# Performance work log

Hardware: AMD Instinct MI355X
Metric: run time of the kernel (lower is better)

Reference implementation:

```python
import jax, jax.numpy as jnp
import numpy as np

HEADS = 16
DIM_HEAD = 64
RMS_EPS = 1.1920929e-07  # torch.finfo(float32).eps (torch RMSNorm eps=None default)
ROPE_THETA = 10000.0


def _rope(x):
    # x: [b, h, n, d]; rotary-embedding-torch style interleaved rotation
    n, d = x.shape[-2], x.shape[-1]
    inv_freq = 1.0 / (ROPE_THETA ** (jnp.arange(0, d, 2, dtype=jnp.float32) / d))
    t = jnp.arange(n, dtype=jnp.float32)
    freqs = t[:, None] * inv_freq[None, :]              # [n, d/2]
    cos = jnp.repeat(jnp.cos(freqs), 2, axis=-1)        # [n, d] interleaved
    sin = jnp.repeat(jnp.sin(freqs), 2, axis=-1)
    x1 = x[..., ::2]
    x2 = x[..., 1::2]
    rot = jnp.stack((-x2, x1), axis=-1).reshape(x.shape)  # rotate_half, interleaved pairs
    return x * cos + rot * sin


def setup_inputs() -> dict:
    key = jax.random.key(0)
    ks = jax.random.split(key, 6)
    b, n, dim = 2, 2048, 1024
    tokens = jax.random.normal(ks[0], (b, n, dim), dtype=jnp.float32)
    norm_weight = jnp.ones((dim,), dtype=jnp.float32)
    wq = jax.random.normal(ks[1], (dim, dim), dtype=jnp.float32) * 0.02
    wk = jax.random.normal(ks[2], (dim, dim), dtype=jnp.float32) * 0.02
    wv = jax.random.normal(ks[3], (dim, dim), dtype=jnp.float32) * 0.02
    wo = jax.random.normal(ks[4], (dim, dim), dtype=jnp.float32) * 0.02
    return {"tokens": tokens, "norm_weight": norm_weight, "wq": wq, "wk": wk, "wv": wv, "wo": wo}


def reference(tokens, norm_weight, wq, wk, wv, wo):
    b, n, dim = tokens.shape
    # RMSNorm (elementwise affine)
    x = tokens * jax.lax.rsqrt(jnp.mean(tokens * tokens, axis=-1, keepdims=True) + RMS_EPS)
    x = x * norm_weight
    # QKV projections (torch Linear: x @ W.T), split heads: b n (h d) -> b h n d
    def split(y):
        return y.reshape(b, n, HEADS, DIM_HEAD).transpose(0, 2, 1, 3)
    q = split(x @ wq.T) * (DIM_HEAD ** -0.5)
    k = split(x @ wk.T)
    v = split(x @ wv.T)
    # rotary embedding (no kv cache -> same positions for q and k)
    q = _rope(q)
    k = _rope(k)
    sim = jnp.einsum('bhid,bhjd->bhij', q, k)
    causal = jnp.triu(jnp.ones((n, n), dtype=bool), k=1)
    sim = jnp.where(causal, -jnp.finfo(sim.dtype).max, sim)
    attn = jax.nn.softmax(sim, axis=-1)
    out = jnp.einsum('bhij,bhjd->bhid', attn, v)
    out = out.transpose(0, 2, 1, 3).reshape(b, n, dim)  # merge heads
    return out @ wo.T
```

## Files before the change

kernel.cpp:

```cpp
#include <hip/hip_runtime.h>

typedef __bf16 bf16x8 __attribute__((ext_vector_type(8)));
typedef float f32x4 __attribute__((ext_vector_type(4)));

#define DIM 1024
#define NSEQ 2048

#define GL2LDS(g, l) __builtin_amdgcn_global_load_lds( \
    (const __attribute__((address_space(1))) void*)(g), \
    (__attribute__((address_space(3))) void*)(l), 16, 0, 0)

#define MFMA16(a, b, c) __builtin_amdgcn_mfma_f32_16x16x32_bf16(a, b, c, 0, 0, 0)

__global__ __launch_bounds__(256) void cvt_kernel(const float* __restrict__ s,
                                                  __bf16* __restrict__ d) {
    int i = (blockIdx.x * 256 + threadIdx.x) * 4;
    float4 f = *(const float4*)(s + i);
    union { uint2 u; __bf16 h[4]; } p;
    p.h[0] = (__bf16)f.x; p.h[1] = (__bf16)f.y;
    p.h[2] = (__bf16)f.z; p.h[3] = (__bf16)f.w;
    *(uint2*)(d + i) = p.u;
}

__global__ __launch_bounds__(256) void cvt3_kernel(const float* __restrict__ wq,
                                                   const float* __restrict__ wk,
                                                   const float* __restrict__ wv,
                                                   __bf16* __restrict__ dq,
                                                   __bf16* __restrict__ dk,
                                                   __bf16* __restrict__ dv,
                                                   int* __restrict__ counters) {
    if (blockIdx.x == 0 && blockIdx.y == 0 && threadIdx.x < 8)
        counters[threadIdx.x] = 0;
    const float* s = blockIdx.y == 0 ? wq : (blockIdx.y == 1 ? wk : wv);
    __bf16*      d = blockIdx.y == 0 ? dq : (blockIdx.y == 1 ? dk : dv);
    int i = (blockIdx.x * 256 + threadIdx.x) * 4;
    float4 f = *(const float4*)(s + i);
    union { uint2 u; __bf16 h[4]; } p;
    p.h[0] = (__bf16)f.x; p.h[1] = (__bf16)f.y;
    p.h[2] = (__bf16)f.z; p.h[3] = (__bf16)f.w;
    *(uint2*)(d + i) = p.u;
}

__global__ __launch_bounds__(256) void rmsnorm_kernel(const float* __restrict__ x,
                                                      const float* __restrict__ g,
                                                      __bf16* __restrict__ o) {
    int row = blockIdx.x;
    int t = threadIdx.x;
    float4 xv = ((const float4*)(x + (size_t)row * DIM))[t];
    float ss = xv.x*xv.x + xv.y*xv.y + xv.z*xv.z + xv.w*xv.w;
    #pragma unroll
    for (int off = 32; off; off >>= 1) ss += __shfl_xor(ss, off, 64);
    __shared__ float red[4];
    if ((t & 63) == 0) red[t >> 6] = ss;
    __syncthreads();
    ss = red[0] + red[1] + red[2] + red[3];
    float r = rsqrtf(ss * (1.0f / 1024.0f) + 1.1920929e-07f);
    float4 gv = ((const float4*)g)[t];
    union { uint2 u; __bf16 h[4]; } p;
    p.h[0] = (__bf16)(xv.x * r * gv.x);
    p.h[1] = (__bf16)(xv.y * r * gv.y);
    p.h[2] = (__bf16)(xv.z * r * gv.z);
    p.h[3] = (__bf16)(xv.w * r * gv.w);
    *(uint2*)(o + (size_t)row * DIM + t * 4) = p.u;
}

__global__ __launch_bounds__(256) void rope_kernel(__bf16* __restrict__ qb,
                                                   __bf16* __restrict__ kb) {
    int bid = blockIdx.x;
    __bf16* x = (bid & 1) ? kb : qb;
    int gid = (bid >> 1) * 256 + threadIdx.x;
    int row = gid >> 9;
    int pr = gid & 511;
    int pos = row & (NSEQ - 1);
    int dp = pr & 31;
    float inv = __expf(-(float)dp * (9.210340371976184f / 32.0f));
    float ang = (float)pos * inv;
    float sn, cs;
    sincosf(ang, &sn, &cs);
    size_t off = (size_t)row * DIM + pr * 2;
    union { unsigned int u; __bf16 h[2]; } p;
    p.u = *(const unsigned int*)(x + off);
    float x1 = (float)p.h[0], x2 = (float)p.h[1];
    p.h[0] = (__bf16)(x1 * cs - x2 * sn);
    p.h[1] = (__bf16)(x2 * cs + x1 * sn);
    *(unsigned int*)(x + off) = p.u;
}

template <typename CT>
__device__ __forceinline__ void gemm_body(const __bf16* __restrict__ A,
                                          const __bf16* __restrict__ B,
                                          CT* __restrict__ C,
                                          int mb, int nb, int ldc, float scale,
                                          __bf16* As, __bf16* Bs) {
    int t = threadIdx.x;
    int w = t >> 6, l = t & 63;
    int wm = (w >> 1) * 64, wn = (w & 1) * 64;
    int lrow = l & 15, lq = l >> 4;
    f32x4 acc[4][4] = {};

    int srow = w * 32 + (l >> 3);
    int sc8 = (l & 7) * 8;
    const __bf16* gA = A + (size_t)(mb * 128 + srow) * 1024 + sc8;
    const __bf16* gB = B + (size_t)(nb * 128 + srow) * 1024 + sc8;
    __bf16* lA = As + (size_t)(w * 32) * 64;
    __bf16* lB = Bs + (size_t)(w * 32) * 64;

    for (int kt = 0; kt < 16; ++kt) {
        int k0 = kt * 64;
        #pragma unroll
        for (int c = 0; c < 4; ++c) {
            GL2LDS(gA + (size_t)c * 8 * 1024 + k0, lA + c * 8 * 64);
            GL2LDS(gB + (size_t)c * 8 * 1024 + k0, lB + c * 8 * 64);
        }
        __syncthreads();
        #pragma unroll
        for (int ch = 0; ch < 2; ++ch) {
            bf16x8 af[4], bfr[4];
            #pragma unroll
            for (int i = 0; i < 4; ++i)
                af[i] = *(const bf16x8*)&As[(wm + i * 16 + lrow) * 64 + ch * 32 + lq * 8];
            #pragma unroll
            for (int i = 0; i < 4; ++i)
                bfr[i] = *(const bf16x8*)&Bs[(wn + i * 16 + lrow) * 64 + ch * 32 + lq * 8];
            #pragma unroll
            for (int rt = 0; rt < 4; ++rt)
                #pragma unroll
                for (int ct = 0; ct < 4; ++ct)
                    acc[rt][ct] = MFMA16(af[rt], bfr[ct], acc[rt][ct]);
        }
        __syncthreads();
    }
    #pragma unroll
    for (int rt = 0; rt < 4; ++rt)
        #pragma unroll
        for (int ct = 0; ct < 4; ++ct)
            #pragma unroll
            for (int r = 0; r < 4; ++r) {
                int row = mb * 128 + wm + rt * 16 + lq * 4 + r;
                int col = nb * 128 + wn + ct * 16 + lrow;
                C[(size_t)row * ldc + col] = (CT)(acc[rt][ct][r] * scale);
            }
}

__global__ __launch_bounds__(256) void qkv_kernel(const __bf16* __restrict__ x,
                                                  const __bf16* __restrict__ wq,
                                                  const __bf16* __restrict__ wk,
                                                  const __bf16* __restrict__ wv,
                                                  __bf16* __restrict__ qb,
                                                  __bf16* __restrict__ kb,
                                                  __bf16* __restrict__ vtb) {
    __shared__ __bf16 As[128 * 64];
    __shared__ __bf16 Bs[128 * 64];
    int bm = blockIdx.x, bn = blockIdx.y, z = blockIdx.z;
    if (z == 0)      gemm_body<__bf16>(x,  wq, qb,  bm, bn, 1024,
                                       0.125f * 1.44269504088896340736f, As, Bs);
    else if (z == 1) gemm_body<__bf16>(x,  wk, kb,  bm, bn, 1024, 1.0f,   As, Bs);
    else             gemm_body<__bf16>(wv, x,  vtb, bn, bm, 4096, 1.0f,   As, Bs);
}

__global__ __launch_bounds__(256) void wo_kernel(const __bf16* __restrict__ A,
                                                 const __bf16* __restrict__ B,
                                                 float* __restrict__ C) {
    __shared__ __bf16 As[128 * 64];
    __shared__ __bf16 Bs[128 * 64];
    gemm_body<float>(A, B, C, blockIdx.x, blockIdx.y, 1024, 1.0f, As, Bs);
}

__global__ __launch_bounds__(256) void attn_kernel(const __bf16* __restrict__ q,
                                                   const __bf16* __restrict__ kk,
                                                   const __bf16* __restrict__ vt,
                                                   __bf16* __restrict__ o,
                                                   int* __restrict__ counters) {
    int xcd = blockIdx.x & 7;
    int t = threadIdx.x;
    int w = t >> 6, l = t & 63;
    int lrow = l & 15, lq = l >> 4;

    __shared__ __bf16 Ps[4][32 * 76];
    __bf16* pw = Ps[w];

    for (;;) {
        int it = 0;
        if (l == 0) it = atomicAdd(&counters[xcd], 1);
        it = __shfl(it, 0, 64);
        if (it >= 256) break;
        int qq = 63 - (it >> 2);
        int bh = xcd * 4 + (it & 3);
        int h = bh & 15;
        int b = bh >> 4;
        int rowbase = b * NSEQ;
        int JT = qq >> 1;

        const __bf16* kbase = kk + (size_t)rowbase * DIM + h * 64;
        const __bf16* vbase = vt + (size_t)(h * 64) * 4096 + b * 2048;

        bf16x8 qf[2][2];
        #pragma unroll
        for (int g = 0; g < 2; ++g) {
            const __bf16* qp = q + (size_t)(rowbase + qq * 32 + g * 16 + lrow) * DIM + h * 64;
            qf[g][0] = *(const bf16x8*)(qp + lq * 8);
            qf[g][1] = *(const bf16x8*)(qp + 32 + lq * 8);
        }

        f32x4 oacc[2][4] = {};
        float m_r[2] = {-1e30f, -1e30f};
        float l_r[2] = {0.0f, 0.0f};

        bf16x8 kA[8], kB[8], vA[8], vB[8];
        #pragma unroll
        for (int ct = 0; ct < 4; ++ct) {
            const __bf16* kp = kbase + (size_t)(ct * 16 + lrow) * DIM;
            kA[ct * 2]     = *(const bf16x8*)(kp + lq * 8);
            kA[ct * 2 + 1] = *(const bf16x8*)(kp + 32 + lq * 8);
            const __bf16* vp = vbase + (size_t)(ct * 16 + lrow) * 4096;
            vA[ct * 2]     = *(const bf16x8*)(vp + lq * 8);
            vA[ct * 2 + 1] = *(const bf16x8*)(vp + 32 + lq * 8);
        }

        auto trip = [&](bf16x8 (&kc)[8], bf16x8 (&kn)[8],
                        bf16x8 (&vc)[8], bf16x8 (&vn)[8], int jt) {
            f32x4 st[2][4];
            #pragma unroll
            for (int ct = 0; ct < 4; ++ct)
                #pragma unroll
                for (int g = 0; g < 2; ++g) {
                    f32x4 z = {};
                    z = MFMA16(kc[ct * 2],     qf[g][0], z);
                    z = MFMA16(kc[ct * 2 + 1], qf[g][1], z);
                    st[g][ct] = z;
                }
            if (jt < JT) {
                int j1 = (jt + 1) * 64;
                #pragma unroll
                for (int ct = 0; ct < 4; ++ct) {
                    const __bf16* kp = kbase + (size_t)(j1 + ct * 16 + lrow) * DIM;
                    kn[ct * 2]     = *(const bf16x8*)(kp + lq * 8);
                    kn[ct * 2 + 1] = *(const bf16x8*)(kp + 32 + lq * 8);
                    const __bf16* vp = vbase + (size_t)(ct * 16 + lrow) * 4096 + j1;
                    vn[ct * 2]     = *(const bf16x8*)(vp + lq * 8);
                    vn[ct * 2 + 1] = *(const bf16x8*)(vp + 32 + lq * 8);
                }
            }
            if (jt == JT) {
                #pragma unroll
                for (int g = 0; g < 2; ++g) {
                    int qr = qq * 32 + g * 16 + lrow - JT * 64;
                    #pragma unroll
                    for (int ct = 0; ct < 4; ++ct)
                        #pragma unroll
                        for (int r = 0; r < 4; ++r)
                            if (ct * 16 + lq * 4 + r > qr) st[g][ct][r] = -3.0e38f;
                }
            }
            #pragma unroll
            for (int g = 0; g < 2; ++g) {
                float m0 = fmaxf(fmaxf(st[g][0][0], st[g][0][1]), fmaxf(st[g][0][2], st[g][0][3]));
                float m1 = fmaxf(fmaxf(st[g][1][0], st[g][1][1]), fmaxf(st[g][1][2], st[g][1][3]));
                float m2 = fmaxf(fmaxf(st[g][2][0], st[g][2][1]), fmaxf(st[g][2][2], st[g][2][3]));
                float m3 = fmaxf(fmaxf(st[g][3][0], st[g][3][1]), fmaxf(st[g][3][2], st[g][3][3]));
                float mx = fmaxf(fmaxf(m0, m1), fmaxf(m2, m3));
                mx = fmaxf(mx, __shfl_xor(mx, 16, 64));
                mx = fmaxf(mx, __shfl_xor(mx, 32, 64));
                if (!__all(mx - m_r[g] <= 8.0f)) {
                    float mnew = fmaxf(m_r[g], mx);
                    float alpha = __builtin_amdgcn_exp2f(m_r[g] - mnew);
                    l_r[g] *= alpha;
                    #pragma unroll
                    for (int ct = 0; ct < 4; ++ct)
                        #pragma unroll
                        for (int r = 0; r < 4; ++r) oacc[g][ct][r] *= alpha;
                    m_r[g] = mnew;
                }
                float ps = 0.0f;
                #pragma unroll
                for (int ct = 0; ct < 4; ++ct)
                    #pragma unroll
                    for (int r = 0; r < 4; ++r) {
                        float p = __builtin_amdgcn_exp2f(st[g][ct][r] - m_r[g]);
                        st[g][ct][r] = p;
                        ps += p;
                    }
                ps += __shfl_xor(ps, 16, 64);
                ps += __shfl_xor(ps, 32, 64);
                l_r[g] += ps;
            }
            #pragma unroll
            for (int g = 0; g < 2; ++g)
                #pragma unroll
                for (int ct = 0; ct < 4; ++ct) {
                    union { uint2 u; __bf16 h4[4]; } pk;
                    #pragma unroll
                    for (int r = 0; r < 4; ++r) pk.h4[r] = (__bf16)st[g][ct][r];
                    *(uint2*)&pw[(g * 16 + lrow) * 76 + ct * 16 + lq * 4] = pk.u;
                }
            bf16x8 pb[2][2];
            #pragma unroll
            for (int g = 0; g < 2; ++g) {
                pb[g][0] = *(const bf16x8*)&pw[(g * 16 + lrow) * 76 + lq * 8];
                pb[g][1] = *(const bf16x8*)&pw[(g * 16 + lrow) * 76 + 32 + lq * 8];
            }
            #pragma unroll
            for (int ct = 0; ct < 4; ++ct)
                #pragma unroll
                for (int g = 0; g < 2; ++g) {
                    oacc[g][ct] = MFMA16(vc[ct * 2],     pb[g][0], oacc[g][ct]);
                    oacc[g][ct] = MFMA16(vc[ct * 2 + 1], pb[g][1], oacc[g][ct]);
                }
        };

        int jt = 0;
        for (;;) {
            trip(kA, kB, vA, vB, jt);
            if (jt == JT) break;
            ++jt;
            trip(kB, kA, vB, vA, jt);
            if (jt == JT) break;
            ++jt;
        }

        #pragma unroll
        for (int g = 0; g < 2; ++g) {
            float rcp = 1.0f / l_r[g];
            const size_t orow = (size_t)(rowbase + qq * 32 + g * 16 + lrow) * DIM + h * 64;
            #pragma unroll
            for (int ct = 0; ct < 4; ++ct) {
                union { uint2 u; __bf16 h4[4]; } pk;
                #pragma unroll
                for (int r = 0; r < 4; ++r) pk.h4[r] = (__bf16)(oacc[g][ct][r] * rcp);
                *(uint2*)(o + orow + ct * 16 + lq * 4) = pk.u;
            }
        }
    }
}

extern "C" void kernel_launch(void* const* d_in, const int* in_sizes, int n_in,
                              void* d_out, int out_size, void* d_ws, size_t ws_size,
                              hipStream_t stream) {
    const float* tokens = (const float*)d_in[0];
    const float* gamma  = (const float*)d_in[1];
    const float* wq = (const float*)d_in[2];
    const float* wk = (const float*)d_in[3];
    const float* wv = (const float*)d_in[4];
    const float* wo = (const float*)d_in[5];

    __bf16* ws  = (__bf16*)d_ws;
    __bf16* x   = ws;
    __bf16* qb  = x   + (size_t)4096 * 1024;
    __bf16* kb  = qb  + (size_t)4096 * 1024;
    __bf16* vtb = kb  + (size_t)4096 * 1024;
    __bf16* ao  = x;
    __bf16* wob = qb;
    float*  out = (float*)d_out;

    __bf16* wqb = (__bf16*)d_out;
    __bf16* wkb = wqb + (size_t)1024 * 1024;
    __bf16* wvb = wkb + (size_t)1024 * 1024;
    int* counters = (int*)((char*)d_out + (size_t)8 * 1024 * 1024);

    cvt3_kernel<<<dim3(1024, 3), 256, 0, stream>>>(wq, wk, wv, wqb, wkb, wvb, counters);

    rmsnorm_kernel<<<4096, 256, 0, stream>>>(tokens, gamma, x);

    qkv_kernel<<<dim3(32, 8, 3), 256, 0, stream>>>(x, wqb, wkb, wvb, qb, kb, vtb);

    rope_kernel<<<16384, 256, 0, stream>>>(qb, kb);

    attn_kernel<<<256, 256, 0, stream>>>(qb, kb, vtb, ao, counters);

    cvt_kernel<<<1024, 256, 0, stream>>>(wo, wob);

    wo_kernel<<<dim3(32, 8), 256, 0, stream>>>(ao, wob, out);
}
```

Before: 239.0 us.

## Share K/V tiles across four waves via double-buffered LDS in attention

The attention kernel now processes 128 query rows per work item, with the four waves sharing one 64-key K/V tile. The tile is staged cooperatively into double-buffered shared memory with register prefetch, replacing the old per-wave scheme where each wave loaded K/V straight from global memory into registers for its own 32 query rows. This cuts global/L2 traffic for K and V by a factor of four and lowers register pressure. In exchange it adds block-wide barriers each iteration, LDS reads for the MFMA operands, coarser work items (64 per XCD instead of 256) and masking over two diagonal tiles.

```diff
diff --git a/kernel.cpp b/kernel.cpp
--- a/kernel.cpp
+++ b/kernel.cpp
@@ -175,21 +175,26 @@
     int t = threadIdx.x;
     int w = t >> 6, l = t & 63;
     int lrow = l & 15, lq = l >> 4;
-
+    int row0 = t >> 3;
+    int c8 = (t & 7) * 8;
+
+    __shared__ __bf16 Kt[2][64 * 72];
+    __shared__ __bf16 Vs[2][64 * 72];
     __shared__ __bf16 Ps[4][32 * 76];
+    __shared__ int s_item;
     __bf16* pw = Ps[w];
 
     for (;;) {
-        int it = 0;
-        if (l == 0) it = atomicAdd(&counters[xcd], 1);
-        it = __shfl(it, 0, 64);
-        if (it >= 256) break;
-        int qq = 63 - (it >> 2);
-        int bh = xcd * 4 + (it & 3);
+        if (t == 0) s_item = atomicAdd(&counters[xcd], 1);
+        __syncthreads();
+        int item = s_item;
+        if (item >= 64) break;
+        int qt = 15 - (item >> 2);
+        int bh = xcd * 4 + (item & 3);
         int h = bh & 15;
         int b = bh >> 4;
         int rowbase = b * NSEQ;
-        int JT = qq >> 1;
+        int JT = 2 * qt + 1;
 
         const __bf16* kbase = kk + (size_t)rowbase * DIM + h * 64;
         const __bf16* vbase = vt + (size_t)(h * 64) * 4096 + b * 2048;
@@ -197,7 +202,7 @@
         bf16x8 qf[2][2];
         #pragma unroll
         for (int g = 0; g < 2; ++g) {
-            const __bf16* qp = q + (size_t)(rowbase + qq * 32 + g * 16 + lrow) * DIM + h * 64;
+            const __bf16* qp = q + (size_t)(rowbase + qt * 128 + w * 32 + g * 16 + lrow) * DIM + h * 64;
             qf[g][0] = *(const bf16x8*)(qp + lq * 8);
             qf[g][1] = *(const bf16x8*)(qp + 32 + lq * 8);
         }
@@ -206,50 +211,48 @@
         float m_r[2] = {-1e30f, -1e30f};
         float l_r[2] = {0.0f, 0.0f};
 
-        bf16x8 kA[8], kB[8], vA[8], vB[8];
-        #pragma unroll
-        for (int ct = 0; ct < 4; ++ct) {
-            const __bf16* kp = kbase + (size_t)(ct * 16 + lrow) * DIM;
-            kA[ct * 2]     = *(const bf16x8*)(kp + lq * 8);
-            kA[ct * 2 + 1] = *(const bf16x8*)(kp + 32 + lq * 8);
-            const __bf16* vp = vbase + (size_t)(ct * 16 + lrow) * 4096;
-            vA[ct * 2]     = *(const bf16x8*)(vp + lq * 8);
-            vA[ct * 2 + 1] = *(const bf16x8*)(vp + 32 + lq * 8);
-        }
-
-        auto trip = [&](bf16x8 (&kc)[8], bf16x8 (&kn)[8],
-                        bf16x8 (&vc)[8], bf16x8 (&vn)[8], int jt) {
+        uint4 kr0, kr1, vr0, vr1;
+        kr0 = *(const uint4*)(kbase + (size_t)row0 * DIM + c8);
+        kr1 = *(const uint4*)(kbase + (size_t)(row0 + 32) * DIM + c8);
+        vr0 = *(const uint4*)(vbase + (size_t)row0 * 4096 + c8);
+        vr1 = *(const uint4*)(vbase + (size_t)(row0 + 32) * 4096 + c8);
+        *(uint4*)&Kt[0][row0 * 72 + c8] = kr0;
+        *(uint4*)&Kt[0][(row0 + 32) * 72 + c8] = kr1;
+        *(uint4*)&Vs[0][row0 * 72 + c8] = vr0;
+        *(uint4*)&Vs[0][(row0 + 32) * 72 + c8] = vr1;
+        __syncthreads();
+
+        for (int jt = 0; jt <= JT; ++jt) {
+            int cur = jt & 1;
+            if (jt < JT) {
+                int j0 = (jt + 1) * 64;
+                kr0 = *(const uint4*)(kbase + (size_t)(j0 + row0) * DIM + c8);
+                kr1 = *(const uint4*)(kbase + (size_t)(j0 + row0 + 32) * DIM + c8);
+                vr0 = *(const uint4*)(vbase + (size_t)row0 * 4096 + j0 + c8);
+                vr1 = *(const uint4*)(vbase + (size_t)(row0 + 32) * 4096 + j0 + c8);
+            }
             f32x4 st[2][4];
             #pragma unroll
-            for (int ct = 0; ct < 4; ++ct)
+            for (int ct = 0; ct < 4; ++ct) {
+                bf16x8 ka0 = *(const bf16x8*)&Kt[cur][(ct * 16 + lrow) * 72 + lq * 8];
+                bf16x8 ka1 = *(const bf16x8*)&Kt[cur][(ct * 16 + lrow) * 72 + 32 + lq * 8];
                 #pragma unroll
                 for (int g = 0; g < 2; ++g) {
                     f32x4 z = {};
-                    z = MFMA16(kc[ct * 2],     qf[g][0], z);
-                    z = MFMA16(kc[ct * 2 + 1], qf[g][1], z);
+                    z = MFMA16(ka0, qf[g][0], z);
+                    z = MFMA16(ka1, qf[g][1], z);
                     st[g][ct] = z;
                 }
-            if (jt < JT) {
-                int j1 = (jt + 1) * 64;
-                #pragma unroll
-                for (int ct = 0; ct < 4; ++ct) {
-                    const __bf16* kp = kbase + (size_t)(j1 + ct * 16 + lrow) * DIM;
-                    kn[ct * 2]     = *(const bf16x8*)(kp + lq * 8);
-                    kn[ct * 2 + 1] = *(const bf16x8*)(kp + 32 + lq * 8);
-                    const __bf16* vp = vbase + (size_t)(ct * 16 + lrow) * 4096 + j1;
-                    vn[ct * 2]     = *(const bf16x8*)(vp + lq * 8);
-                    vn[ct * 2 + 1] = *(const bf16x8*)(vp + 32 + lq * 8);
-                }
-            }
-            if (jt == JT) {
+            }
+            if (jt >= JT - 1) {
                 #pragma unroll
                 for (int g = 0; g < 2; ++g) {
-                    int qr = qq * 32 + g * 16 + lrow - JT * 64;
+                    int qrel = qt * 128 + w * 32 + g * 16 + lrow - jt * 64;
                     #pragma unroll
                     for (int ct = 0; ct < 4; ++ct)
                         #pragma unroll
                         for (int r = 0; r < 4; ++r)
-                            if (ct * 16 + lq * 4 + r > qr) st[g][ct][r] = -3.0e38f;
+                            if (ct * 16 + lq * 4 + r > qrel) st[g][ct][r] = -3.0e38f;
                 }
             }
             #pragma unroll
@@ -300,28 +303,27 @@
                 pb[g][1] = *(const bf16x8*)&pw[(g * 16 + lrow) * 76 + 32 + lq * 8];
             }
             #pragma unroll
-            for (int ct = 0; ct < 4; ++ct)
+            for (int ct = 0; ct < 4; ++ct) {
+                bf16x8 va0 = *(const bf16x8*)&Vs[cur][(ct * 16 + lrow) * 72 + lq * 8];
+                bf16x8 va1 = *(const bf16x8*)&Vs[cur][(ct * 16 + lrow) * 72 + 32 + lq * 8];
                 #pragma unroll
                 for (int g = 0; g < 2; ++g) {
-                    oacc[g][ct] = MFMA16(vc[ct * 2],     pb[g][0], oacc[g][ct]);
-                    oacc[g][ct] = MFMA16(vc[ct * 2 + 1], pb[g][1], oacc[g][ct]);
-                }
-        };
-
-        int jt = 0;
-        for (;;) {
-            trip(kA, kB, vA, vB, jt);
-            if (jt == JT) break;
-            ++jt;
-            trip(kB, kA, vB, vA, jt);
-            if (jt == JT) break;
-            ++jt;
-        }
-
+                    oacc[g][ct] = MFMA16(va0, pb[g][0], oacc[g][ct]);
+                    oacc[g][ct] = MFMA16(va1, pb[g][1], oacc[g][ct]);
+                }
+            }
+            if (jt < JT) {
+                *(uint4*)&Kt[cur ^ 1][row0 * 72 + c8] = kr0;
+                *(uint4*)&Kt[cur ^ 1][(row0 + 32) * 72 + c8] = kr1;
+                *(uint4*)&Vs[cur ^ 1][row0 * 72 + c8] = vr0;
+                *(uint4*)&Vs[cur ^ 1][(row0 + 32) * 72 + c8] = vr1;
+            }
+            __syncthreads();
+        }
         #pragma unroll
         for (int g = 0; g < 2; ++g) {
             float rcp = 1.0f / l_r[g];
-            const size_t orow = (size_t)(rowbase + qq * 32 + g * 16 + lrow) * DIM + h * 64;
+            const size_t orow = (size_t)(rowbase + qt * 128 + w * 32 + g * 16 + lrow) * DIM + h * 64;
             #pragma unroll
             for (int ct = 0; ct < 4; ++ct) {
                 union { uint2 u; __bf16 h4[4]; } pk;
```

After: 234.5 us. About the same (-1.9%).
